# Kernel optimization log

Measured on AMD Instinct MI355X. Metric: run time of the kernel, lower is better.

## Reference

```python
import jax, jax.numpy as jnp
import numpy as np

B, S, C, H = 2, 4096, 512, 8
D = C // H  # per-head depth


def setup_inputs() -> dict:
    key = jax.random.key(0)
    ks = jax.random.split(key, 12)
    scale = 1.0 / np.sqrt(C)
    inp = {
        "q": jax.random.normal(ks[0], (B, S, C), jnp.float32),
        "k": jax.random.normal(ks[1], (B, S, C), jnp.float32),
        "v": jax.random.normal(ks[2], (B, S, C), jnp.float32),
        "mask": jax.random.randint(ks[3], (1, 1, S, S), 0, 2).astype(jnp.float32),
        "wq": jax.random.normal(ks[4], (C, C), jnp.float32) * scale,
        "bq": jnp.zeros((C,), jnp.float32),
        "wk": jax.random.normal(ks[5], (C, C), jnp.float32) * scale,
        "bk": jnp.zeros((C,), jnp.float32),
        "wv": jax.random.normal(ks[6], (C, C), jnp.float32) * scale,
        "bv": jnp.zeros((C,), jnp.float32),
        "wo": jax.random.normal(ks[7], (C, C), jnp.float32) * scale,
        "bo": jnp.zeros((C,), jnp.float32),
    }
    return inp


def _split_heads(x):
    # [B,S,C] -> [B,H,S,D]
    b, s, _ = x.shape
    return x.reshape(b, s, H, D).transpose(0, 2, 1, 3)


def reference(q, k, v, mask, wq, bq, wk, bk, wv, bv, wo, bo):
    # torch Linear: y = x @ W.T + b
    qh = _split_heads(q @ wq.T + bq)  # [B,H,S,D]
    kh = _split_heads(k @ wk.T + bk)
    vh = _split_heads(v @ wv.T + bv)

    # scaled dot-product attention with additive legacy mask
    scores = jnp.einsum("bhqd,bhkd->bhqk", qh, kh) / jnp.sqrt(jnp.float32(D))
    scores = scores + mask * jnp.float32(-1e12)
    attn = jax.nn.softmax(scores, axis=-1)  # [B,H,Sq,Sk]
    out_h = jnp.einsum("bhqk,bhkd->bhqd", attn, vh)  # [B,H,S,D]

    # merge heads and output projection
    concat = out_h.transpose(0, 2, 1, 3).reshape(q.shape[0], -1, C)
    out = concat @ wo.T + bo  # [B,S,C]
    return out, attn
```

## Files before the change

kernel.cpp:

```cpp
#include <hip/hip_runtime.h>
#include <hip/hip_bf16.h>
#include <cstdint>

#define SB 4096
#define CB 512
#define HB 8
#define DB 64
#define BB 2

#define QSCALE 0.18033688011112042f

typedef __attribute__((ext_vector_type(8))) short s16x8;
typedef __attribute__((ext_vector_type(4))) short s16x4;
typedef __attribute__((ext_vector_type(4))) float f32x4;

__device__ __forceinline__ short f2bf(float f) {
    union { float f; unsigned int u; } v; v.f = f;
    unsigned int r = v.u + 0x7fffu + ((v.u >> 16) & 1u);
    return (short)(r >> 16);
}

__device__ __forceinline__ unsigned int cvtpk(float lo, float hi) {
    unsigned int r;
    asm("v_cvt_pk_bf16_f32 %0, %1, %2" : "=v"(r) : "v"(lo), "v"(hi));
    return r;
}

__device__ __forceinline__ f32x4 mfma16(s16x8 a, s16x8 b, f32x4 c) {
    return __builtin_amdgcn_mfma_f32_16x16x32_bf16(a, b, c, 0, 0, 0);
}

__device__ __forceinline__ f32x4 mfma16x16(s16x4 a, s16x4 b, f32x4 c) {
    asm("v_mfma_f32_16x16x16_bf16 %0, %1, %2, %0" : "+v"(c) : "v"(a), "v"(b));
    return c;
}

__global__ __launch_bounds__(256) void qkv_mask_kernel(
    const float* __restrict__ q, const float* __restrict__ k, const float* __restrict__ v,
    const float* __restrict__ wq, const float* __restrict__ wk, const float* __restrict__ wv,
    const float* __restrict__ bq, const float* __restrict__ bk, const float* __restrict__ bv,
    unsigned short* __restrict__ Qh, unsigned short* __restrict__ Kh,
    unsigned short* __restrict__ Vt,
    const float* __restrict__ mask, unsigned long long* __restrict__ bits)
{
    const int z = blockIdx.z;
    if (z >= 3) {
        size_t idx = (((size_t)(z - 3) * 512) + blockIdx.y * 64 + blockIdx.x) * 256
                     + threadIdx.x;
        float mv = mask[idx];
        unsigned long long bmask = __ballot(mv != 0.0f);
        if ((threadIdx.x & 63) == 0) bits[idx >> 6] = bmask;
        return;
    }

    const float* X = (z == 0) ? q : (z == 1) ? k : v;
    const float* W = (z == 0) ? wq : (z == 1) ? wk : wv;
    const float* bias = (z == 0) ? bq : (z == 1) ? bk : bv;
    unsigned short* dst = (z == 0) ? Qh : (z == 1) ? Kh : Vt;
    const float oscale = (z == 0) ? QSCALE : 1.0f;
    const int which = (z == 2) ? 2 : 0;

    __shared__ __align__(16) short As[128 * 40];
    __shared__ __align__(16) short Bs[64 * 40];
    const int t = threadIdx.x;
    const int w = t >> 6, lane = t & 63, g = lane >> 4, c = lane & 15;
    const int wr = w >> 1, wc = w & 1;
    const int m0 = blockIdx.x * 128, n0 = blockIdx.y * 64;

    f32x4 acc[4][2];
#pragma unroll
    for (int i = 0; i < 4; ++i)
#pragma unroll
        for (int j = 0; j < 2; ++j) acc[i][j] = (f32x4){0.f, 0.f, 0.f, 0.f};

    for (int k0 = 0; k0 < CB; k0 += 32) {
        __syncthreads();
#pragma unroll
        for (int i = 0; i < 4; ++i) {
            int idx = t + i * 256; int r = idx >> 3, c4 = idx & 7;
            float4 vv = *(const float4*)(X + (size_t)(m0 + r) * CB + k0 + c4 * 4);
            s16x4 p; p[0] = f2bf(vv.x); p[1] = f2bf(vv.y); p[2] = f2bf(vv.z); p[3] = f2bf(vv.w);
            *(s16x4*)&As[r * 40 + c4 * 4] = p;
        }
#pragma unroll
        for (int i = 0; i < 2; ++i) {
            int idx = t + i * 256; int r = idx >> 3, c4 = idx & 7;
            float4 vv = *(const float4*)(W + (size_t)(n0 + r) * CB + k0 + c4 * 4);
            s16x4 p; p[0] = f2bf(vv.x); p[1] = f2bf(vv.y); p[2] = f2bf(vv.z); p[3] = f2bf(vv.w);
            *(s16x4*)&Bs[r * 40 + c4 * 4] = p;
        }
        __syncthreads();
        const int koff = g * 8;
        s16x8 a[4], bb[2];
#pragma unroll
        for (int mf = 0; mf < 4; ++mf)
            a[mf] = *(const s16x8*)&As[(wr * 64 + mf * 16 + c) * 40 + koff];
#pragma unroll
        for (int nf = 0; nf < 2; ++nf)
            bb[nf] = *(const s16x8*)&Bs[(wc * 32 + nf * 16 + c) * 40 + koff];
#pragma unroll
        for (int mf = 0; mf < 4; ++mf)
#pragma unroll
            for (int nf = 0; nf < 2; ++nf)
                acc[mf][nf] = mfma16(a[mf], bb[nf], acc[mf][nf]);
    }

#pragma unroll
    for (int nf = 0; nf < 2; ++nf) {
        const int n = n0 + wc * 32 + nf * 16 + c;
        const float bv2 = bias[n];
        const int h = n >> 6, d = n & 63;
#pragma unroll
        for (int mf = 0; mf < 4; ++mf) {
#pragma unroll
            for (int r = 0; r < 4; ++r) {
                int m = m0 + wr * 64 + mf * 16 + g * 4 + r;
                float val = (acc[mf][nf][r] + bv2) * oscale;
                int b = m >> 12, s = m & (SB - 1);
                size_t off;
                if (which == 0) off = (((size_t)(b * HB + h)) * SB + s) * DB + d;
                else            off = (((size_t)(b * HB + h)) * DB + d) * SB + s;
                dst[off] = (unsigned short)f2bf(val);
            }
        }
    }
}

__global__ __launch_bounds__(512) void flash_kernel(
    const unsigned short* __restrict__ Qh, const unsigned short* __restrict__ Kh,
    const unsigned short* __restrict__ Vt, const unsigned long long* __restrict__ mbits,
    unsigned short* __restrict__ concat, float* __restrict__ invbuf)
{
    __shared__ __align__(16) short Klds[2][64 * 64];
    __shared__ __align__(16) short Vlds[2][64 * 64];

    const int t = threadIdx.x, w = t >> 6, lane = t & 63, g = lane >> 4, c = lane & 15;
    const int bid = blockIdx.x;
    const int xcd = bid & 7, idx = bid >> 3;
    const int bh = xcd * 2 + (idx >> 5);
    const int qb = idx & 31;
    const int b = bh >> 3, h = bh & 7;
    const int i0 = qb * 128;

    const unsigned short* Qbase = Qh + ((size_t)bh * SB + i0 + w * 16) * DB;
    const unsigned short* Kbase = Kh + (size_t)bh * SB * DB;
    const unsigned short* Vbase = Vt + (size_t)bh * DB * SB;

    s16x8 qf[2];
#pragma unroll
    for (int ks = 0; ks < 2; ++ks)
        qf[ks] = *(const s16x8*)(Qbase + (size_t)c * DB + ks * 32 + g * 8);

    const int qrow = i0 + w * 16 + c;
    const size_t mrowbase = (size_t)qrow * (SB / 64);
    float rowacc = 0.f;
    f32x4 acc[4];
#pragma unroll
    for (int df = 0; df < 4; ++df) acc[df] = (f32x4){0.f, 0.f, 0.f, 0.f};

    const int sr = t >> 3;
    const int colb = (t & 7) * 16;
    const int swz = (sr & 7) << 4;

    s16x8 kreg, vreg;

    auto LOAD = [&](int j0) {
        kreg = *(const s16x8*)((const char*)(Kbase + (size_t)(j0 + sr) * DB) + colb);
        vreg = *(const s16x8*)((const char*)(Vbase + (size_t)sr * SB + j0) + colb);
    };
    auto STORE = [&](int buf) {
        *(s16x8*)((char*)&Klds[buf][0] + sr * 128 + (colb ^ swz)) = kreg;
        *(s16x8*)((char*)&Vlds[buf][0] + sr * 128 + (colb ^ swz)) = vreg;
    };
    auto COMPUTE = [&](int buf, unsigned long long mw64) {
        f32x4 sc[4];
        __builtin_amdgcn_s_setprio(1);
#pragma unroll
        for (int jf = 0; jf < 4; ++jf) {
            sc[jf] = (f32x4){0.f, 0.f, 0.f, 0.f};
#pragma unroll
            for (int ks = 0; ks < 2; ++ks) {
                s16x8 kf = *(const s16x8*)((char*)&Klds[buf][0] + (jf * 16 + c) * 128 +
                                           ((ks * 64 + g * 16) ^ ((c & 7) << 4)));
                sc[jf] = mfma16(kf, qf[ks], sc[jf]);
            }
        }
        __builtin_amdgcn_s_setprio(0);

        const unsigned long long mw = mw64 >> (g * 4);
        const unsigned int nib[4] = {
            (unsigned int)mw & 0xFu, (unsigned int)(mw >> 16) & 0xFu,
            (unsigned int)(mw >> 32) & 0xFu, (unsigned int)(mw >> 48) & 0xFu };

        s16x4 pf4[4];
#pragma unroll
        for (int jf = 0; jf < 4; ++jf) {
            float e[4];
#pragma unroll
            for (int r = 0; r < 4; ++r)
                e[r] = ((nib[jf] >> r) & 1u) ? 0.f : __builtin_amdgcn_exp2f(sc[jf][r]);
            rowacc += (e[0] + e[1]) + (e[2] + e[3]);
            union { unsigned int u[2]; s16x4 v; } pk;
            pk.u[0] = cvtpk(e[0], e[1]);
            pk.u[1] = cvtpk(e[2], e[3]);
            pf4[jf] = pk.v;
        }

        __builtin_amdgcn_s_setprio(1);
#pragma unroll
        for (int df = 0; df < 4; ++df) {
#pragma unroll
            for (int jf = 0; jf < 4; ++jf) {
                s16x4 vf = *(const s16x4*)((char*)&Vlds[buf][0] + (df * 16 + c) * 128 +
                                           ((jf * 32 + g * 8) ^ ((c & 7) << 4)));
                acc[df] = mfma16x16(pf4[jf], vf, acc[df]);
            }
        }
        __builtin_amdgcn_s_setprio(0);
    };

    unsigned long long mwcur = mbits[mrowbase];
    LOAD(0);
    STORE(0);
    __syncthreads();
    int cur = 0;
    for (int jt = 0; jt < SB / 64 - 1; ++jt) {
        LOAD((jt + 1) * 64);
        unsigned long long mwnext = mbits[mrowbase + jt + 1];
        COMPUTE(cur, mwcur);
        STORE(cur ^ 1);
        __syncthreads();
        mwcur = mwnext;
        cur ^= 1;
    }
    COMPUTE(cur, mwcur);

    rowacc += __shfl_xor(rowacc, 16);
    rowacc += __shfl_xor(rowacc, 32);
    const float inv = 1.0f / rowacc;
    if (lane < 16) invbuf[(size_t)bh * SB + i0 + w * 16 + c] = inv;

    float ir[4];
#pragma unroll
    for (int r = 0; r < 4; ++r) ir[r] = __shfl(inv, g * 4 + r);

#pragma unroll
    for (int df = 0; df < 4; ++df) {
#pragma unroll
        for (int r = 0; r < 4; ++r) {
            const int s_ = i0 + w * 16 + g * 4 + r;
            concat[(size_t)(b * SB + s_) * CB + h * DB + df * 16 + c] =
                (unsigned short)f2bf(acc[df][r] * ir[r]);
        }
    }
}

__global__ __launch_bounds__(256) void attn_final_kernel(
    const unsigned short* __restrict__ Qh, const unsigned short* __restrict__ Kh,
    const unsigned long long* __restrict__ mbits, const float* __restrict__ invbuf,
    float* __restrict__ attnO,
    const unsigned short* __restrict__ Ain, const float* __restrict__ W,
    const float* __restrict__ bias, float* __restrict__ out)
{
    if (blockIdx.z == 16) {
        __shared__ __align__(16) short As[128 * 40];
        __shared__ __align__(16) short Bs[64 * 40];
        const int t = threadIdx.x;
        const int w = t >> 6, lane = t & 63, g = lane >> 4, c = lane & 15;
        const int wr = w >> 1, wc = w & 1;
        const int m0 = blockIdx.x * 128, n0 = blockIdx.y * 64;

        f32x4 acc[4][2];
#pragma unroll
        for (int i = 0; i < 4; ++i)
#pragma unroll
            for (int j = 0; j < 2; ++j) acc[i][j] = (f32x4){0.f, 0.f, 0.f, 0.f};

        for (int k0 = 0; k0 < CB; k0 += 32) {
            __syncthreads();
#pragma unroll
            for (int i = 0; i < 2; ++i) {
                int idx = t + i * 256; int r = idx >> 2, ch = idx & 3;
                *(s16x8*)&As[r * 40 + ch * 8] =
                    *(const s16x8*)(Ain + (size_t)(m0 + r) * CB + k0 + ch * 8);
            }
#pragma unroll
            for (int i = 0; i < 2; ++i) {
                int idx = t + i * 256; int r = idx >> 3, c4 = idx & 7;
                float4 v = *(const float4*)(W + (size_t)(n0 + r) * CB + k0 + c4 * 4);
                s16x4 p; p[0] = f2bf(v.x); p[1] = f2bf(v.y); p[2] = f2bf(v.z); p[3] = f2bf(v.w);
                *(s16x4*)&Bs[r * 40 + c4 * 4] = p;
            }
            __syncthreads();
            const int koff = g * 8;
            s16x8 a[4], bb[2];
#pragma unroll
            for (int mf = 0; mf < 4; ++mf)
                a[mf] = *(const s16x8*)&As[(wr * 64 + mf * 16 + c) * 40 + koff];
#pragma unroll
            for (int nf = 0; nf < 2; ++nf)
                bb[nf] = *(const s16x8*)&Bs[(wc * 32 + nf * 16 + c) * 40 + koff];
#pragma unroll
            for (int mf = 0; mf < 4; ++mf)
#pragma unroll
                for (int nf = 0; nf < 2; ++nf)
                    acc[mf][nf] = mfma16(a[mf], bb[nf], acc[mf][nf]);
        }

#pragma unroll
        for (int nf = 0; nf < 2; ++nf) {
            const int n = n0 + wc * 32 + nf * 16 + c;
            const float bv = bias[n];
#pragma unroll
            for (int mf = 0; mf < 4; ++mf) {
#pragma unroll
                for (int r = 0; r < 4; ++r) {
                    int m = m0 + wr * 64 + mf * 16 + g * 4 + r;
                    out[(size_t)m * CB + n] = acc[mf][nf][r] + bv;
                }
            }
        }
        return;
    }

    __shared__ __align__(16) float TP[4][16 * 64];

    const int t = threadIdx.x, w = t >> 6, lane = t & 63, g = lane >> 4, c = lane & 15;
    const int q0 = blockIdx.x * 64;
    const int ks0 = blockIdx.y * 512 + w * 128;
    const size_t bh = blockIdx.z;
    const unsigned short* Qb_ = Qh + (bh * SB + q0) * DB;
    const unsigned short* Kb_ = Kh + bh * SB * DB;
    float* aO = attnO + bh * (size_t)SB * SB;
    char* tp = (char*)&TP[w][0];

    s16x8 qf[4][2];
    float invv[4];
    size_t mrb[4];
#pragma unroll
    for (int qi = 0; qi < 4; ++qi) {
#pragma unroll
        for (int ks = 0; ks < 2; ++ks)
            qf[qi][ks] = *(const s16x8*)(Qb_ + (size_t)(qi * 16 + c) * DB + ks * 32 + g * 8);
        invv[qi] = invbuf[bh * SB + q0 + qi * 16 + c];
        mrb[qi] = (size_t)(q0 + qi * 16 + c) * (SB / 64);
    }

#pragma unroll
    for (int kc = 0; kc < 2; ++kc) {
        const int kch = ks0 + kc * 64;
        s16x8 kf[4][2];
#pragma unroll
        for (int jf = 0; jf < 4; ++jf)
#pragma unroll
            for (int ks = 0; ks < 2; ++ks)
                kf[jf][ks] = *(const s16x8*)(Kb_ + (size_t)(kch + jf * 16 + c) * DB + ks * 32 + g * 8);

#pragma unroll
        for (int qi = 0; qi < 4; ++qi) {
            f32x4 sc[4];
#pragma unroll
            for (int jf = 0; jf < 4; ++jf) {
                sc[jf] = (f32x4){0.f, 0.f, 0.f, 0.f};
#pragma unroll
                for (int ks = 0; ks < 2; ++ks)
                    sc[jf] = mfma16(kf[jf][ks], qf[qi][ks], sc[jf]);
            }
            unsigned long long mw = mbits[mrb[qi] + (kch >> 6)] >> (g * 4);
            const unsigned int nib[4] = {
                (unsigned int)mw & 0xFu, (unsigned int)(mw >> 16) & 0xFu,
                (unsigned int)(mw >> 32) & 0xFu, (unsigned int)(mw >> 48) & 0xFu };
            const float iv = invv[qi];

#pragma unroll
            for (int jf = 0; jf < 4; ++jf) {
                f32x4 o;
#pragma unroll
                for (int r = 0; r < 4; ++r)
                    o[r] = ((nib[jf] >> r) & 1u) ? 0.f : __builtin_amdgcn_exp2f(sc[jf][r]) * iv;
                *(f32x4*)(tp + c * 256 + ((jf * 64 + g * 16) ^ (c << 4))) = o;
            }

            const size_t gbase = (size_t)(q0 + qi * 16) * SB + kch;
#pragma unroll
            for (int i = 0; i < 4; ++i) {
                const int rr = i * 4 + g;
                f32x4 vv = *(const f32x4*)(tp + rr * 256 + ((c * 16) ^ (rr << 4)));
                __builtin_nontemporal_store(vv, (f32x4*)(aO + gbase + (size_t)rr * SB + c * 4));
            }
        }
    }
}

extern "C" void kernel_launch(void* const* d_in, const int* in_sizes, int n_in,
                              void* d_out, int out_size, void* d_ws, size_t ws_size,
                              hipStream_t stream) {
    const float* q    = (const float*)d_in[0];
    const float* k    = (const float*)d_in[1];
    const float* v    = (const float*)d_in[2];
    const float* mask = (const float*)d_in[3];
    const float* wq   = (const float*)d_in[4];
    const float* bq   = (const float*)d_in[5];
    const float* wk   = (const float*)d_in[6];
    const float* bk   = (const float*)d_in[7];
    const float* wv   = (const float*)d_in[8];
    const float* bv   = (const float*)d_in[9];
    const float* wo   = (const float*)d_in[10];
    const float* bo   = (const float*)d_in[11];

    const size_t NE = (size_t)BB * HB * SB * DB;
    unsigned short* Qh     = (unsigned short*)d_ws;
    unsigned short* Kh     = Qh + NE;
    unsigned short* Vt     = Kh + NE;
    unsigned short* concat = Vt + NE;
    unsigned long long* mbits = (unsigned long long*)((char*)d_ws + 4 * NE * sizeof(unsigned short));
    float* invbuf = (float*)((char*)d_ws + 4 * NE * sizeof(unsigned short) + (size_t)SB * SB / 8);

    float* outp  = (float*)d_out;
    float* attnp = outp + (size_t)BB * SB * CB;

    qkv_mask_kernel<<<dim3(64, 8, 131), 256, 0, stream>>>(
        q, k, v, wq, wk, wv, bq, bk, bv, Qh, Kh, Vt, mask, mbits);
    flash_kernel<<<dim3(512, 1, 1), 512, 0, stream>>>(Qh, Kh, Vt, mbits, concat, invbuf);
    attn_final_kernel<<<dim3(SB / 64, 8, HB * BB + 1), 256, 0, stream>>>(
        Qh, Kh, mbits, invbuf, attnp, concat, wo, bo, outp);
}
```

Before: 415.3 us.

## Fuse attention-probability output into flash kernel and split output projection

The flash kernel now uses 256-thread blocks covering 64 query rows (1024 blocks). After computing the row sum, each block does a second pass over all keys to recompute the scores and write the normalized attention matrix directly. This removes the invbuf round trip and the separate attention-writing kernel. The output projection becomes its own kernel launched afterwards, so it no longer overlaps with the attention writes. Each block now re-reads K straight from global memory in the second pass, and the attention-matrix write is serialized behind the flash computation within each block.

```diff
diff --git a/kernel.cpp b/kernel.cpp
--- a/kernel.cpp
+++ b/kernel.cpp
@@ -126,21 +126,20 @@
     }
 }
 
-__global__ __launch_bounds__(512) void flash_kernel(
+__global__ __launch_bounds__(256) void fused_attn_kernel(
     const unsigned short* __restrict__ Qh, const unsigned short* __restrict__ Kh,
     const unsigned short* __restrict__ Vt, const unsigned long long* __restrict__ mbits,
-    unsigned short* __restrict__ concat, float* __restrict__ invbuf)
+    unsigned short* __restrict__ concat, float* __restrict__ attnO)
 {
-    __shared__ __align__(16) short Klds[2][64 * 64];
-    __shared__ __align__(16) short Vlds[2][64 * 64];
+    __shared__ __align__(16) char smem[32768];
 
     const int t = threadIdx.x, w = t >> 6, lane = t & 63, g = lane >> 4, c = lane & 15;
     const int bid = blockIdx.x;
     const int xcd = bid & 7, idx = bid >> 3;
-    const int bh = xcd * 2 + (idx >> 5);
-    const int qb = idx & 31;
+    const int bh = xcd * 2 + (idx >> 6);
+    const int qb = idx & 63;
     const int b = bh >> 3, h = bh & 7;
-    const int i0 = qb * 128;
+    const int i0 = qb * 64;
 
     const unsigned short* Qbase = Qh + ((size_t)bh * SB + i0 + w * 16) * DB;
     const unsigned short* Kbase = Kh + (size_t)bh * SB * DB;
@@ -158,19 +157,26 @@
 #pragma unroll
     for (int df = 0; df < 4; ++df) acc[df] = (f32x4){0.f, 0.f, 0.f, 0.f};
 
-    const int sr = t >> 3;
-    const int colb = (t & 7) * 16;
+    const int sr = t >> 2, sq = t & 3;
     const int swz = (sr & 7) << 4;
 
-    s16x8 kreg, vreg;
+    s16x8 kreg[2], vreg[2];
 
     auto LOAD = [&](int j0) {
-        kreg = *(const s16x8*)((const char*)(Kbase + (size_t)(j0 + sr) * DB) + colb);
-        vreg = *(const s16x8*)((const char*)(Vbase + (size_t)sr * SB + j0) + colb);
+#pragma unroll
+        for (int i = 0; i < 2; ++i) {
+            const int colb = sq * 16 + i * 64;
+            kreg[i] = *(const s16x8*)((const char*)(Kbase + (size_t)(j0 + sr) * DB) + colb);
+            vreg[i] = *(const s16x8*)((const char*)(Vbase + (size_t)sr * SB + j0) + colb);
+        }
     };
     auto STORE = [&](int buf) {
-        *(s16x8*)((char*)&Klds[buf][0] + sr * 128 + (colb ^ swz)) = kreg;
-        *(s16x8*)((char*)&Vlds[buf][0] + sr * 128 + (colb ^ swz)) = vreg;
+#pragma unroll
+        for (int i = 0; i < 2; ++i) {
+            const int colb = sq * 16 + i * 64;
+            *(s16x8*)(smem + buf * 8192 + sr * 128 + (colb ^ swz)) = kreg[i];
+            *(s16x8*)(smem + 16384 + buf * 8192 + sr * 128 + (colb ^ swz)) = vreg[i];
+        }
     };
     auto COMPUTE = [&](int buf, unsigned long long mw64) {
         f32x4 sc[4];
@@ -180,7 +186,7 @@
             sc[jf] = (f32x4){0.f, 0.f, 0.f, 0.f};
 #pragma unroll
             for (int ks = 0; ks < 2; ++ks) {
-                s16x8 kf = *(const s16x8*)((char*)&Klds[buf][0] + (jf * 16 + c) * 128 +
+                s16x8 kf = *(const s16x8*)(smem + buf * 8192 + (jf * 16 + c) * 128 +
                                            ((ks * 64 + g * 16) ^ ((c & 7) << 4)));
                 sc[jf] = mfma16(kf, qf[ks], sc[jf]);
             }
@@ -211,7 +217,7 @@
         for (int df = 0; df < 4; ++df) {
 #pragma unroll
             for (int jf = 0; jf < 4; ++jf) {
-                s16x4 vf = *(const s16x4*)((char*)&Vlds[buf][0] + (df * 16 + c) * 128 +
+                s16x4 vf = *(const s16x4*)(smem + 16384 + buf * 8192 + (df * 16 + c) * 128 +
                                            ((jf * 32 + g * 8) ^ ((c & 7) << 4)));
                 acc[df] = mfma16x16(pf4[jf], vf, acc[df]);
             }
@@ -238,7 +244,6 @@
     rowacc += __shfl_xor(rowacc, 16);
     rowacc += __shfl_xor(rowacc, 32);
     const float inv = 1.0f / rowacc;
-    if (lane < 16) invbuf[(size_t)bh * SB + i0 + w * 16 + c] = inv;
 
     float ir[4];
 #pragma unroll
@@ -253,140 +258,112 @@
                 (unsigned short)f2bf(acc[df][r] * ir[r]);
         }
     }
-}
-
-__global__ __launch_bounds__(256) void attn_final_kernel(
-    const unsigned short* __restrict__ Qh, const unsigned short* __restrict__ Kh,
-    const unsigned long long* __restrict__ mbits, const float* __restrict__ invbuf,
-    float* __restrict__ attnO,
+
+    __syncthreads();
+
+    char* tp = smem + w * 4096;
+    float* aO = attnO + (size_t)bh * SB * SB;
+    const size_t rowbase = (size_t)(i0 + w * 16) * SB;
+    const float iv = inv;
+
+    for (int kt = 0; kt < SB / 64; ++kt) {
+        const int kch = kt * 64;
+        s16x8 kf[4][2];
+#pragma unroll
+        for (int jf = 0; jf < 4; ++jf)
+#pragma unroll
+            for (int ks = 0; ks < 2; ++ks)
+                kf[jf][ks] = *(const s16x8*)(Kbase + (size_t)(kch + jf * 16 + c) * DB + ks * 32 + g * 8);
+
+        f32x4 sc[4];
+#pragma unroll
+        for (int jf = 0; jf < 4; ++jf) {
+            sc[jf] = (f32x4){0.f, 0.f, 0.f, 0.f};
+#pragma unroll
+            for (int ks = 0; ks < 2; ++ks)
+                sc[jf] = mfma16(kf[jf][ks], qf[ks], sc[jf]);
+        }
+        unsigned long long mw = mbits[mrowbase + kt] >> (g * 4);
+        const unsigned int nib[4] = {
+            (unsigned int)mw & 0xFu, (unsigned int)(mw >> 16) & 0xFu,
+            (unsigned int)(mw >> 32) & 0xFu, (unsigned int)(mw >> 48) & 0xFu };
+
+#pragma unroll
+        for (int jf = 0; jf < 4; ++jf) {
+            f32x4 o;
+#pragma unroll
+            for (int r = 0; r < 4; ++r)
+                o[r] = ((nib[jf] >> r) & 1u) ? 0.f : __builtin_amdgcn_exp2f(sc[jf][r]) * iv;
+            *(f32x4*)(tp + c * 256 + ((jf * 64 + g * 16) ^ (c << 4))) = o;
+        }
+
+#pragma unroll
+        for (int i = 0; i < 4; ++i) {
+            const int rr = i * 4 + g;
+            f32x4 vv = *(const f32x4*)(tp + rr * 256 + ((c * 16) ^ (rr << 4)));
+            __builtin_nontemporal_store(vv, (f32x4*)(aO + rowbase + (size_t)rr * SB + kch + c * 4));
+        }
+    }
+}
+
+__global__ __launch_bounds__(256) void final_kernel(
     const unsigned short* __restrict__ Ain, const float* __restrict__ W,
     const float* __restrict__ bias, float* __restrict__ out)
 {
-    if (blockIdx.z == 16) {
-        __shared__ __align__(16) short As[128 * 40];
-        __shared__ __align__(16) short Bs[64 * 40];
-        const int t = threadIdx.x;
-        const int w = t >> 6, lane = t & 63, g = lane >> 4, c = lane & 15;
-        const int wr = w >> 1, wc = w & 1;
-        const int m0 = blockIdx.x * 128, n0 = blockIdx.y * 64;
-
-        f32x4 acc[4][2];
-#pragma unroll
-        for (int i = 0; i < 4; ++i)
-#pragma unroll
-            for (int j = 0; j < 2; ++j) acc[i][j] = (f32x4){0.f, 0.f, 0.f, 0.f};
-
-        for (int k0 = 0; k0 < CB; k0 += 32) {
-            __syncthreads();
-#pragma unroll
-            for (int i = 0; i < 2; ++i) {
-                int idx = t + i * 256; int r = idx >> 2, ch = idx & 3;
-                *(s16x8*)&As[r * 40 + ch * 8] =
-                    *(const s16x8*)(Ain + (size_t)(m0 + r) * CB + k0 + ch * 8);
-            }
-#pragma unroll
-            for (int i = 0; i < 2; ++i) {
-                int idx = t + i * 256; int r = idx >> 3, c4 = idx & 7;
-                float4 v = *(const float4*)(W + (size_t)(n0 + r) * CB + k0 + c4 * 4);
-                s16x4 p; p[0] = f2bf(v.x); p[1] = f2bf(v.y); p[2] = f2bf(v.z); p[3] = f2bf(v.w);
-                *(s16x4*)&Bs[r * 40 + c4 * 4] = p;
-            }
-            __syncthreads();
-            const int koff = g * 8;
-            s16x8 a[4], bb[2];
-#pragma unroll
-            for (int mf = 0; mf < 4; ++mf)
-                a[mf] = *(const s16x8*)&As[(wr * 64 + mf * 16 + c) * 40 + koff];
+    __shared__ __align__(16) short As[128 * 40];
+    __shared__ __align__(16) short Bs[64 * 40];
+    const int t = threadIdx.x;
+    const int w = t >> 6, lane = t & 63, g = lane >> 4, c = lane & 15;
+    const int wr = w >> 1, wc = w & 1;
+    const int m0 = blockIdx.x * 128, n0 = blockIdx.y * 64;
+
+    f32x4 acc[4][2];
+#pragma unroll
+    for (int i = 0; i < 4; ++i)
+#pragma unroll
+        for (int j = 0; j < 2; ++j) acc[i][j] = (f32x4){0.f, 0.f, 0.f, 0.f};
+
+    for (int k0 = 0; k0 < CB; k0 += 32) {
+        __syncthreads();
+#pragma unroll
+        for (int i = 0; i < 2; ++i) {
+            int idx = t + i * 256; int r = idx >> 2, ch = idx & 3;
+            *(s16x8*)&As[r * 40 + ch * 8] =
+                *(const s16x8*)(Ain + (size_t)(m0 + r) * CB + k0 + ch * 8);
+        }
+#pragma unroll
+        for (int i = 0; i < 2; ++i) {
+            int idx = t + i * 256; int r = idx >> 3, c4 = idx & 7;
+            float4 v = *(const float4*)(W + (size_t)(n0 + r) * CB + k0 + c4 * 4);
+            s16x4 p; p[0] = f2bf(v.x); p[1] = f2bf(v.y); p[2] = f2bf(v.z); p[3] = f2bf(v.w);
+            *(s16x4*)&Bs[r * 40 + c4 * 4] = p;
+        }
+        __syncthreads();
+        const int koff = g * 8;
+        s16x8 a[4], bb[2];
+#pragma unroll
+        for (int mf = 0; mf < 4; ++mf)
+            a[mf] = *(const s16x8*)&As[(wr * 64 + mf * 16 + c) * 40 + koff];
+#pragma unroll
+        for (int nf = 0; nf < 2; ++nf)
+            bb[nf] = *(const s16x8*)&Bs[(wc * 32 + nf * 16 + c) * 40 + koff];
+#pragma unroll
+        for (int mf = 0; mf < 4; ++mf)
 #pragma unroll
             for (int nf = 0; nf < 2; ++nf)
-                bb[nf] = *(const s16x8*)&Bs[(wc * 32 + nf * 16 + c) * 40 + koff];
-#pragma unroll
-            for (int mf = 0; mf < 4; ++mf)
-#pragma unroll
-                for (int nf = 0; nf < 2; ++nf)
-                    acc[mf][nf] = mfma16(a[mf], bb[nf], acc[mf][nf]);
-        }
-
-#pragma unroll
-        for (int nf = 0; nf < 2; ++nf) {
-            const int n = n0 + wc * 32 + nf * 16 + c;
-            const float bv = bias[n];
-#pragma unroll
-            for (int mf = 0; mf < 4; ++mf) {
-#pragma unroll
-                for (int r = 0; r < 4; ++r) {
-                    int m = m0 + wr * 64 + mf * 16 + g * 4 + r;
-                    out[(size_t)m * CB + n] = acc[mf][nf][r] + bv;
-                }
-            }
-        }
-        return;
-    }
-
-    __shared__ __align__(16) float TP[4][16 * 64];
-
-    const int t = threadIdx.x, w = t >> 6, lane = t & 63, g = lane >> 4, c = lane & 15;
-    const int q0 = blockIdx.x * 64;
-    const int ks0 = blockIdx.y * 512 + w * 128;
-    const size_t bh = blockIdx.z;
-    const unsigned short* Qb_ = Qh + (bh * SB + q0) * DB;
-    const unsigned short* Kb_ = Kh + bh * SB * DB;
-    float* aO = attnO + bh * (size_t)SB * SB;
-    char* tp = (char*)&TP[w][0];
-
-    s16x8 qf[4][2];
-    float invv[4];
-    size_t mrb[4];
-#pragma unroll
-    for (int qi = 0; qi < 4; ++qi) {
-#pragma unroll
-        for (int ks = 0; ks < 2; ++ks)
-            qf[qi][ks] = *(const s16x8*)(Qb_ + (size_t)(qi * 16 + c) * DB + ks * 32 + g * 8);
-        invv[qi] = invbuf[bh * SB + q0 + qi * 16 + c];
-        mrb[qi] = (size_t)(q0 + qi * 16 + c) * (SB / 64);
-    }
-
-#pragma unroll
-    for (int kc = 0; kc < 2; ++kc) {
-        const int kch = ks0 + kc * 64;
-        s16x8 kf[4][2];
-#pragma unroll
-        for (int jf = 0; jf < 4; ++jf)
-#pragma unroll
-            for (int ks = 0; ks < 2; ++ks)
-                kf[jf][ks] = *(const s16x8*)(Kb_ + (size_t)(kch + jf * 16 + c) * DB + ks * 32 + g * 8);
-
-#pragma unroll
-        for (int qi = 0; qi < 4; ++qi) {
-            f32x4 sc[4];
-#pragma unroll
-            for (int jf = 0; jf < 4; ++jf) {
-                sc[jf] = (f32x4){0.f, 0.f, 0.f, 0.f};
-#pragma unroll
-                for (int ks = 0; ks < 2; ++ks)
-                    sc[jf] = mfma16(kf[jf][ks], qf[qi][ks], sc[jf]);
-            }
-            unsigned long long mw = mbits[mrb[qi] + (kch >> 6)] >> (g * 4);
-            const unsigned int nib[4] = {
-                (unsigned int)mw & 0xFu, (unsigned int)(mw >> 16) & 0xFu,
-                (unsigned int)(mw >> 32) & 0xFu, (unsigned int)(mw >> 48) & 0xFu };
-            const float iv = invv[qi];
-
-#pragma unroll
-            for (int jf = 0; jf < 4; ++jf) {
-                f32x4 o;
-#pragma unroll
-                for (int r = 0; r < 4; ++r)
-                    o[r] = ((nib[jf] >> r) & 1u) ? 0.f : __builtin_amdgcn_exp2f(sc[jf][r]) * iv;
-                *(f32x4*)(tp + c * 256 + ((jf * 64 + g * 16) ^ (c << 4))) = o;
-            }
-
-            const size_t gbase = (size_t)(q0 + qi * 16) * SB + kch;
-#pragma unroll
-            for (int i = 0; i < 4; ++i) {
-                const int rr = i * 4 + g;
-                f32x4 vv = *(const f32x4*)(tp + rr * 256 + ((c * 16) ^ (rr << 4)));
-                __builtin_nontemporal_store(vv, (f32x4*)(aO + gbase + (size_t)rr * SB + c * 4));
+                acc[mf][nf] = mfma16(a[mf], bb[nf], acc[mf][nf]);
+    }
+
+#pragma unroll
+    for (int nf = 0; nf < 2; ++nf) {
+        const int n = n0 + wc * 32 + nf * 16 + c;
+        const float bv = bias[n];
+#pragma unroll
+        for (int mf = 0; mf < 4; ++mf) {
+#pragma unroll
+            for (int r = 0; r < 4; ++r) {
+                int m = m0 + wr * 64 + mf * 16 + g * 4 + r;
+                out[(size_t)m * CB + n] = acc[mf][nf][r] + bv;
             }
         }
     }
@@ -414,14 +391,13 @@
     unsigned short* Vt     = Kh + NE;
     unsigned short* concat = Vt + NE;
     unsigned long long* mbits = (unsigned long long*)((char*)d_ws + 4 * NE * sizeof(unsigned short));
-    float* invbuf = (float*)((char*)d_ws + 4 * NE * sizeof(unsigned short) + (size_t)SB * SB / 8);
 
     float* outp  = (float*)d_out;
     float* attnp = outp + (size_t)BB * SB * CB;
 
     qkv_mask_kernel<<<dim3(64, 8, 131), 256, 0, stream>>>(
         q, k, v, wq, wk, wv, bq, bk, bv, Qh, Kh, Vt, mask, mbits);
-    flash_kernel<<<dim3(512, 1, 1), 512, 0, stream>>>(Qh, Kh, Vt, mbits, concat, invbuf);
-    attn_final_kernel<<<dim3(SB / 64, 8, HB * BB + 1), 256, 0, stream>>>(
-        Qh, Kh, mbits, invbuf, attnp, concat, wo, bo, outp);
-}
+    fused_attn_kernel<<<dim3(1024, 1, 1), 256, 0, stream>>>(
+        Qh, Kh, Vt, mbits, concat, attnp);
+    final_kernel<<<dim3(64, 8, 1), 256, 0, stream>>>(concat, wo, bo, outp);
+}
```

Measured after the change: 485.9 us. +17.0%, slower.
